# Performance work log

Measured on AMD Instinct MI355X. Metric: run time of the kernel, lower is better.

## Reference

```python
import jax, jax.numpy as jnp
import numpy as np
from jax import lax

B, T, IN, H, OUT = 64, 512, 256, 1024, 512

def _uniform(key, shape, std):
    return jax.random.uniform(key, shape, jnp.float32, -std, std)

def setup_inputs() -> dict:
    key = jax.random.key(0)
    ks = jax.random.split(key, 12)
    std = 1.0 / np.sqrt(H)
    return {
        "x": jax.random.normal(ks[0], (B, T, IN), jnp.float32),
        "Wx0": _uniform(ks[1], (H, IN), std), "bx0": _uniform(ks[2], (H,), std),
        "Wh0": _uniform(ks[3], (H, H), std),  "bh0": _uniform(ks[4], (H,), std),
        "Wx1": _uniform(ks[5], (H, H), std),  "bx1": _uniform(ks[6], (H,), std),
        "Wh1": _uniform(ks[7], (H, H), std),  "bh1": _uniform(ks[8], (H,), std),
        "Wfc": _uniform(ks[9], (OUT, H), 1.0 / np.sqrt(H)),
        "bfc": _uniform(ks[10], (OUT,), 1.0 / np.sqrt(H)),
    }

def _run_layer(xs, Wx, bx, Wh, bh):
    # xs: [B, T, D_in] -> hidden sequence [B, T, H]
    xproj = jnp.einsum('btd,hd->bth', xs, Wx) + bx + bh  # precompute input projection
    def step(h, xp):
        h = jnp.tanh(xp + h @ Wh.T)
        return h, h
    h0 = jnp.zeros((xs.shape[0], Wh.shape[0]), xs.dtype)
    _, hs = lax.scan(step, h0, jnp.swapaxes(xproj, 0, 1))  # [T, B, H]
    return jnp.swapaxes(hs, 0, 1)

def reference(x, Wx0, bx0, Wh0, bh0, Wx1, bx1, Wh1, bh1, Wfc, bfc):
    h1 = _run_layer(x, Wx0, bx0, Wh0, bh0)   # layer 0 hidden sequence
    h2 = _run_layer(h1, Wx1, bx1, Wh1, bh1)  # layer 1 hidden sequence
    last = h2[:, -1, :]                       # last timestep of top layer
    return last @ Wfc.T + bfc
```

## Files before the change

kernel.cpp:

```cpp
#include <hip/hip_runtime.h>
#include <hip/hip_bf16.h>

#define Bb   64
#define Tt   512
#define INN  256
#define HH   1024
#define OUTN 512

#define NCOL 32
#define MG   16
#define NGRP (Bb / MG)
#define NSLOT 64
#define FSTR 8

typedef __attribute__((ext_vector_type(8))) short bf16x8;
typedef __attribute__((ext_vector_type(4))) float f32x4;

__device__ __forceinline__ unsigned short f2b(float f) {
  unsigned u = __float_as_uint(f);
  u += 0x7FFFu + ((u >> 16) & 1u);
  return (unsigned short)(u >> 16);
}
__device__ __forceinline__ float b2f(unsigned short u) {
  return __uint_as_float((unsigned)u << 16);
}

__device__ __forceinline__ unsigned int cohLoadU32(const unsigned int* p) {
  return __hip_atomic_load(p, __ATOMIC_RELAXED, __HIP_MEMORY_SCOPE_AGENT);
}
__device__ __forceinline__ unsigned long long cohLoadU64(const unsigned long long* p) {
  return __hip_atomic_load(p, __ATOMIC_RELAXED, __HIP_MEMORY_SCOPE_AGENT);
}
__device__ __forceinline__ unsigned short cohLoadU16(const unsigned short* p) {
  return __hip_atomic_load(p, __ATOMIC_RELAXED, __HIP_MEMORY_SCOPE_AGENT);
}
__device__ __forceinline__ void cohStoreU16(unsigned short* p, unsigned short v) {
  __hip_atomic_store(p, v, __ATOMIC_RELAXED, __HIP_MEMORY_SCOPE_AGENT);
}
__device__ __forceinline__ void cohStoreU32(unsigned int* p, unsigned int v) {
  __hip_atomic_store(p, v, __ATOMIC_RELAXED, __HIP_MEMORY_SCOPE_AGENT);
}

__device__ __forceinline__ f32x4 splat4(float v) { f32x4 r = {v, v, v, v}; return r; }

union U16 { unsigned long long u[2]; bf16x8 v; };

#define ALOADO(d, p, OFF)                                                     \
  asm volatile("global_load_dwordx4 %0, %1, off offset:" #OFF " sc0 sc1"      \
               : "=v"(d) : "v"(p))
#define VMW(N)                                                                \
  do {                                                                        \
    asm volatile("s_waitcnt vmcnt(" #N ")" ::: "memory");                     \
    __builtin_amdgcn_sched_barrier(0);                                        \
  } while (0)

__global__ void cvt4(const float* __restrict__ in, unsigned short* __restrict__ out, int n4) {
  int i = blockIdx.x * blockDim.x + threadIdx.x;
  if (i >= n4) return;
  float4 v = ((const float4*)in)[i];
  ushort4 o;
  o.x = f2b(v.x); o.y = f2b(v.y); o.z = f2b(v.z); o.w = f2b(v.w);
  ((ushort4*)out)[i] = o;
}

__global__ void addv(const float* __restrict__ a, const float* __restrict__ b,
                     float* __restrict__ o, int n) {
  int i = blockIdx.x * blockDim.x + threadIdx.x;
  if (i < n) o[i] = a[i] + b[i];
}

__global__ void zerok(unsigned int* __restrict__ p, int n) {
  int i = blockIdx.x * blockDim.x + threadIdx.x;
  if (i < n) p[i] = 0u;
}

__device__ __forceinline__ void waitflags(const unsigned int* gf, int l, unsigned need) {
#pragma clang loop unroll(disable)
  for (int guard = 0; guard < 4000000; ++guard) {
    unsigned f = cohLoadU32(gf + l * FSTR);
    if (__all((int)(f >= need))) return;
    __builtin_amdgcn_s_sleep(1);
  }
}
__device__ __forceinline__ void waitflag1(const unsigned int* slot, unsigned need) {
#pragma clang loop unroll(disable)
  for (int guard = 0; guard < 4000000; ++guard) {
    if (cohLoadU32(slot) >= need) return;
    __builtin_amdgcn_s_sleep(1);
  }
}

#define ISSUE8(V, O0, O1, O2, O3, O4, O5, O6, O7)                             \
  ALOADO(V##0, Ap, O0); ALOADO(V##1, Ap, O1); ALOADO(V##2, Ap, O2);           \
  ALOADO(V##3, Ap, O3); ALOADO(V##4, Ap, O4); ALOADO(V##5, Ap, O5);           \
  ALOADO(V##6, Ap, O6); ALOADO(V##7, Ap, O7);
#define COMP8(V, WI)                                                          \
  acc  = __builtin_amdgcn_mfma_f32_16x16x32_bf16(V##0, w[(WI)+0], acc,  0,0,0);\
  acc2 = __builtin_amdgcn_mfma_f32_16x16x32_bf16(V##1, w[(WI)+1], acc2, 0,0,0);\
  acc  = __builtin_amdgcn_mfma_f32_16x16x32_bf16(V##2, w[(WI)+2], acc,  0,0,0);\
  acc2 = __builtin_amdgcn_mfma_f32_16x16x32_bf16(V##3, w[(WI)+3], acc2, 0,0,0);\
  acc  = __builtin_amdgcn_mfma_f32_16x16x32_bf16(V##4, w[(WI)+4], acc,  0,0,0);\
  acc2 = __builtin_amdgcn_mfma_f32_16x16x32_bf16(V##5, w[(WI)+5], acc2, 0,0,0);\
  acc  = __builtin_amdgcn_mfma_f32_16x16x32_bf16(V##6, w[(WI)+6], acc,  0,0,0);\
  acc2 = __builtin_amdgcn_mfma_f32_16x16x32_bf16(V##7, w[(WI)+7], acc2, 0,0,0);

__device__ __forceinline__ f32x4 kphase(const short* Ap, bf16x8* w, f32x4 acc) {
#pragma unroll
  for (int c = 0; c < 32; ++c) asm volatile("" : "+a"(w[c]));
  f32x4 acc2 = {0, 0, 0, 0};
  bf16x8 A_0, A_1, A_2, A_3, A_4, A_5, A_6, A_7;
  bf16x8 B_0, B_1, B_2, B_3, B_4, B_5, B_6, B_7;
  bf16x8 C_0, C_1, C_2, C_3, C_4, C_5, C_6, C_7;
  bf16x8 D_0, D_1, D_2, D_3, D_4, D_5, D_6, D_7;
  ISSUE8(A_,    0,   64,  128,  192,  256,  320,  384,  448)
  ISSUE8(B_,  512,  576,  640,  704,  768,  832,  896,  960)
  ISSUE8(C_, 1024, 1088, 1152, 1216, 1280, 1344, 1408, 1472)
  ISSUE8(D_, 1536, 1600, 1664, 1728, 1792, 1856, 1920, 1984)
  VMW(24); COMP8(A_,  0)
  VMW(16); COMP8(B_,  8)
  VMW(8);  COMP8(C_, 16)
  VMW(0);  COMP8(D_, 24)
  return acc + acc2;
}

__global__ __launch_bounds__(128) void rnn3(
    const __hip_bfloat16* __restrict__ xs,
    const __hip_bfloat16* __restrict__ Wx0, const __hip_bfloat16* __restrict__ Wh0,
    const __hip_bfloat16* __restrict__ Wx1, const __hip_bfloat16* __restrict__ Wh1,
    const float* __restrict__ b0s, const float* __restrict__ b1s,
    __hip_bfloat16* __restrict__ P0, __hip_bfloat16* __restrict__ P1,
    unsigned int* flags)
{
  const int tid = threadIdx.x;
  const int l   = tid & 63;
  const int wv  = tid >> 6;
  const int bid = blockIdx.x;
  const int stage = bid % 3;
  const int idx = bid / 3;
  const int j   = idx & 31;
  const int g   = idx >> 5;
  const int n0  = j * NCOL;
  const int rowA = g * MG;
  const int fr = l & 15;
  const int lh = l >> 4;
  const int rb = lh << 2;
  const int ccol = n0 + wv * 16 + fr;

  unsigned int* gf0 = flags + (0 * NGRP + g) * (NSLOT * FSTR);
  unsigned int* gfx = flags + (1 * NGRP + g) * (NSLOT * FSTR);
  unsigned int* gf1 = flags + (2 * NGRP + g) * (NSLOT * FSTR);
  const int wslot = (j * 2 + wv) * FSTR;
  const long laneA = (long)(rowA + fr) * HH + (lh << 3);
  unsigned short* P0u = (unsigned short*)P0;
  unsigned short* P1u = (unsigned short*)P1;

  const short* Wg = (const short*)(stage == 0 ? Wh0 : (stage == 1 ? Wx1 : Wh1));
  const short* Wgrow = Wg + (long)ccol * HH + (lh << 3);
  bf16x8 w[32];
#pragma unroll
  for (int c = 0; c < 32; ++c) w[c] = *(const bf16x8*)(Wgrow + (c << 5));
#pragma unroll
  for (int c = 0; c < 32; ++c) asm volatile("" : "+a"(w[c]));

  if (stage == 0) {
    const float bias = b0s[ccol];
    const short* xrow = (const short*)xs + (long)(rowA + fr) * (Tt * INN) + (lh << 3);
    const short* Wx0row = (const short*)Wx0 + (long)ccol * INN + (lh << 3);
    bf16x8 wx[8];
#pragma unroll
    for (int c = 0; c < 8; ++c) wx[c] = *(const bf16x8*)(Wx0row + (c << 5));
#pragma unroll
    for (int c = 0; c < 8; ++c) asm volatile("" : "+a"(wx[c]));
    f32x4 acc = splat4(bias);
#pragma unroll
    for (int c = 0; c < 8; ++c) {
      bf16x8 a = *(const bf16x8*)(xrow + (c << 5));
      acc = __builtin_amdgcn_mfma_f32_16x16x32_bf16(a, wx[c], acc, 0, 0, 0);
    }
    for (int t = 0; t < Tt; ++t) {
      if (t > 0) {
        waitflags(gf0, l, (unsigned)t);
        acc = kphase((const short*)P0 + (long)(t - 1) * (Bb * HH) + laneA, w, acc);
      }
      const long cb = ((long)t * Bb + rowA + rb) * HH + ccol;
#pragma unroll
      for (int r = 0; r < 4; ++r)
        cohStoreU16(P0u + cb + (long)r * HH, f2b(tanhf(acc[r])));
      asm volatile("s_waitcnt vmcnt(0)" ::: "memory");
      if (l == 0) cohStoreU32(gf0 + wslot, (unsigned)(t + 1));
      if (t + 1 < Tt) {
        acc = splat4(bias);
        const short* xr = xrow + (t + 1) * INN;
#pragma unroll
        for (int c = 0; c < 8; ++c) {
          bf16x8 a = *(const bf16x8*)(xr + (c << 5));
          acc = __builtin_amdgcn_mfma_f32_16x16x32_bf16(a, wx[c], acc, 0, 0, 0);
        }
      }
    }
  } else if (stage == 1) {
    const float bias = b1s[ccol];
    for (int t = 0; t < Tt; ++t) {
      waitflags(gf0, l, (unsigned)(t + 1));
      f32x4 acc = kphase((const short*)P0 + (long)t * (Bb * HH) + laneA, w,
                         splat4(bias));
      const long cb = ((long)t * Bb + rowA + rb) * HH + ccol;
#pragma unroll
      for (int r = 0; r < 4; ++r)
        cohStoreU16(P1u + cb + (long)r * HH, f2b(acc[r]));
      asm volatile("s_waitcnt vmcnt(0)" ::: "memory");
      if (l == 0) cohStoreU32(gfx + wslot, (unsigned)(t + 1));
    }
  } else {
    const unsigned int* myxpf = gfx + wslot;
    for (int t = 0; t < Tt; ++t) {
      waitflag1(myxpf, (unsigned)(t + 1));
      const long cb = ((long)t * Bb + rowA + rb) * HH + ccol;
      float xb[4];
#pragma unroll
      for (int r = 0; r < 4; ++r)
        xb[r] = b2f(cohLoadU16(P1u + cb + (long)r * HH));
      f32x4 acc = {0, 0, 0, 0};
      if (t > 0) {
        waitflags(gf1, l, (unsigned)t);
        acc = kphase((const short*)P1 + (long)(t - 1) * (Bb * HH) + laneA, w, acc);
      }
#pragma unroll
      for (int r = 0; r < 4; ++r)
        cohStoreU16(P1u + cb + (long)r * HH, f2b(tanhf(acc[r] + xb[r])));
      asm volatile("s_waitcnt vmcnt(0)" ::: "memory");
      if (l == 0) cohStoreU32(gf1 + wslot, (unsigned)(t + 1));
    }
  }
}

__global__ void fc_kernel(const __hip_bfloat16* __restrict__ A,
                          const __hip_bfloat16* __restrict__ W,
                          const float* __restrict__ bias,
                          float* __restrict__ C)
{
  const int l   = threadIdx.x;
  const int m0  = blockIdx.x << 4;
  const int n0  = blockIdx.y << 6;
  const int r16 = l & 15;
  const int lh  = l >> 4;

  const unsigned long long* Au =
      (const unsigned long long*)((const short*)A + (long)(m0 + r16) * HH);
  const short* Wp = (const short*)W;
  const long w0 = (long)(n0 + r16) * HH + (lh << 3);
  const long wS = (long)HH << 4;

  f32x4 acc0 = {0,0,0,0}, acc1 = {0,0,0,0}, acc2 = {0,0,0,0}, acc3 = {0,0,0,0};
  for (int kc = 0; kc < HH; kc += 32) {
    U16 a;
    a.u[0] = cohLoadU64(Au + (kc >> 2) + (lh << 1));
    a.u[1] = cohLoadU64(Au + (kc >> 2) + (lh << 1) + 1);
    bf16x8 b0 = *(const bf16x8*)(Wp + w0 +          kc);
    bf16x8 b1 = *(const bf16x8*)(Wp + w0 + wS     + kc);
    bf16x8 b2 = *(const bf16x8*)(Wp + w0 + 2 * wS + kc);
    bf16x8 b3 = *(const bf16x8*)(Wp + w0 + 3 * wS + kc);
    acc0 = __builtin_amdgcn_mfma_f32_16x16x32_bf16(a.v, b0, acc0, 0, 0, 0);
    acc1 = __builtin_amdgcn_mfma_f32_16x16x32_bf16(a.v, b1, acc1, 0, 0, 0);
    acc2 = __builtin_amdgcn_mfma_f32_16x16x32_bf16(a.v, b2, acc2, 0, 0, 0);
    acc3 = __builtin_amdgcn_mfma_f32_16x16x32_bf16(a.v, b3, acc3, 0, 0, 0);
  }
  const int col = l & 15;
  const int rbb = (l >> 4) << 2;
#define FCEP(FIDX, ACC)                                                       \
  { const int n = n0 + (FIDX << 4) + col;                                     \
    _Pragma("unroll")                                                         \
    for (int r = 0; r < 4; ++r)                                               \
      C[(long)(m0 + rbb + r) * OUTN + n] = ACC[r] + bias[n]; }
  FCEP(0, acc0) FCEP(1, acc1) FCEP(2, acc2) FCEP(3, acc3)
#undef FCEP
}

extern "C" void kernel_launch(void* const* d_in, const int* in_sizes, int n_in,
                              void* d_out, int out_size, void* d_ws, size_t ws_size,
                              hipStream_t stream)
{
  const float* x   = (const float*)d_in[0];
  const float* Wx0 = (const float*)d_in[1];
  const float* bx0 = (const float*)d_in[2];
  const float* Wh0 = (const float*)d_in[3];
  const float* bh0 = (const float*)d_in[4];
  const float* Wx1 = (const float*)d_in[5];
  const float* bx1 = (const float*)d_in[6];
  const float* Wh1 = (const float*)d_in[7];
  const float* bh1 = (const float*)d_in[8];
  const float* Wfc = (const float*)d_in[9];
  const float* bfc = (const float*)d_in[10];

  char* ws = (char*)d_ws;
  const long SZ_XBF = (long)Bb * Tt * INN * 2;
  const long SZ_P   = (long)Bb * Tt * HH  * 2;
  __hip_bfloat16* xbf   = (__hip_bfloat16*)(ws);
  __hip_bfloat16* P0    = (__hip_bfloat16*)(ws + SZ_XBF);
  __hip_bfloat16* P1    = (__hip_bfloat16*)(ws + SZ_XBF + SZ_P);
  __hip_bfloat16* Wx0b  = (__hip_bfloat16*)(ws + SZ_XBF + 2 * SZ_P);
  __hip_bfloat16* Wh0b  = (__hip_bfloat16*)((char*)Wx0b + (long)HH * INN * 2);
  __hip_bfloat16* Wx1b  = (__hip_bfloat16*)((char*)Wh0b + (long)HH * HH * 2);
  __hip_bfloat16* Wh1b  = (__hip_bfloat16*)((char*)Wx1b + (long)HH * HH * 2);
  __hip_bfloat16* Wfcb  = (__hip_bfloat16*)((char*)Wh1b + (long)HH * HH * 2);
  float*          b0sum = (float*)((char*)Wfcb + (long)OUTN * HH * 2);
  float*          b1sum = (float*)((char*)b0sum + HH * 4);
  unsigned int*   flg   = (unsigned int*)((char*)b1sum + HH * 4);

  const int FLGN = 3 * NGRP * NSLOT * FSTR;

  {
    int n4;
    n4 = (Bb * Tt * INN) / 4; cvt4<<<(n4 + 255) / 256, 256, 0, stream>>>(x,   (unsigned short*)xbf,  n4);
    n4 = (HH * INN) / 4;      cvt4<<<(n4 + 255) / 256, 256, 0, stream>>>(Wx0, (unsigned short*)Wx0b, n4);
    n4 = (HH * HH) / 4;       cvt4<<<(n4 + 255) / 256, 256, 0, stream>>>(Wh0, (unsigned short*)Wh0b, n4);
    n4 = (HH * HH) / 4;       cvt4<<<(n4 + 255) / 256, 256, 0, stream>>>(Wx1, (unsigned short*)Wx1b, n4);
    n4 = (HH * HH) / 4;       cvt4<<<(n4 + 255) / 256, 256, 0, stream>>>(Wh1, (unsigned short*)Wh1b, n4);
    n4 = (OUTN * HH) / 4;     cvt4<<<(n4 + 255) / 256, 256, 0, stream>>>(Wfc, (unsigned short*)Wfcb, n4);
    addv<<<4, 256, 0, stream>>>(bx0, bh0, b0sum, HH);
    addv<<<4, 256, 0, stream>>>(bx1, bh1, b1sum, HH);
    zerok<<<(FLGN + 255) / 256, 256, 0, stream>>>(flg, FLGN);
  }

  rnn3<<<dim3(384), 128, 0, stream>>>(
      xbf, Wx0b, Wh0b, Wx1b, Wh1b, b0sum, b1sum, P0, P1, flg);

  fc_kernel<<<dim3(Bb / 16, OUTN / 64), 64, 0, stream>>>(
      P1 + (long)(Tt - 1) * Bb * HH, Wfcb, bfc, (float*)d_out);
}
```

Measured before the change: 3.349 ms.

## Widen each wave to 32 output columns, halving the persistent block count

Each wave now computes two 16-column tiles (left and right) and reuses every loaded A fragment for two MFMAs, so it keeps 64 weight fragments resident in AGPRs instead of 32. The grid shrinks from 384 to 192 persistent blocks, the flag slots per group drop to 32, and the wait loops poll only 32 flags. The Wx0 weights are now reloaded from memory on each step rather than kept in registers. The intent is to halve the redundant hidden-state reads and the flag traffic per step. The cost is a longer serial MFMA chain per wave, heavier register pressure, and fewer CUs working on each timestep.

```diff
diff --git a/kernel.cpp b/kernel.cpp
--- a/kernel.cpp
+++ b/kernel.cpp
@@ -7,11 +7,11 @@
 #define HH   1024
 #define OUTN 512
 
-#define NCOL 32
-#define MG   16
-#define NGRP (Bb / MG)
-#define NSLOT 64
-#define FSTR 8
+#define MG    16
+#define NGRP  (Bb / MG)
+#define NBLKG 16
+#define NSLOT 32
+#define FSTR  8
 
 typedef __attribute__((ext_vector_type(8))) short bf16x8;
 typedef __attribute__((ext_vector_type(4))) float f32x4;
@@ -77,7 +77,7 @@
 __device__ __forceinline__ void waitflags(const unsigned int* gf, int l, unsigned need) {
 #pragma clang loop unroll(disable)
   for (int guard = 0; guard < 4000000; ++guard) {
-    unsigned f = cohLoadU32(gf + l * FSTR);
+    unsigned f = cohLoadU32(gf + (l & 31) * FSTR);
     if (__all((int)(f >= need))) return;
     __builtin_amdgcn_s_sleep(1);
   }
@@ -94,20 +94,17 @@
   ALOADO(V##0, Ap, O0); ALOADO(V##1, Ap, O1); ALOADO(V##2, Ap, O2);           \
   ALOADO(V##3, Ap, O3); ALOADO(V##4, Ap, O4); ALOADO(V##5, Ap, O5);           \
   ALOADO(V##6, Ap, O6); ALOADO(V##7, Ap, O7);
+#define C2(V, CH)                                                             \
+  accL = __builtin_amdgcn_mfma_f32_16x16x32_bf16(V, w[2*(CH)],   accL, 0,0,0);\
+  accR = __builtin_amdgcn_mfma_f32_16x16x32_bf16(V, w[2*(CH)+1], accR, 0,0,0);
 #define COMP8(V, WI)                                                          \
-  acc  = __builtin_amdgcn_mfma_f32_16x16x32_bf16(V##0, w[(WI)+0], acc,  0,0,0);\
-  acc2 = __builtin_amdgcn_mfma_f32_16x16x32_bf16(V##1, w[(WI)+1], acc2, 0,0,0);\
-  acc  = __builtin_amdgcn_mfma_f32_16x16x32_bf16(V##2, w[(WI)+2], acc,  0,0,0);\
-  acc2 = __builtin_amdgcn_mfma_f32_16x16x32_bf16(V##3, w[(WI)+3], acc2, 0,0,0);\
-  acc  = __builtin_amdgcn_mfma_f32_16x16x32_bf16(V##4, w[(WI)+4], acc,  0,0,0);\
-  acc2 = __builtin_amdgcn_mfma_f32_16x16x32_bf16(V##5, w[(WI)+5], acc2, 0,0,0);\
-  acc  = __builtin_amdgcn_mfma_f32_16x16x32_bf16(V##6, w[(WI)+6], acc,  0,0,0);\
-  acc2 = __builtin_amdgcn_mfma_f32_16x16x32_bf16(V##7, w[(WI)+7], acc2, 0,0,0);
-
-__device__ __forceinline__ f32x4 kphase(const short* Ap, bf16x8* w, f32x4 acc) {
-#pragma unroll
-  for (int c = 0; c < 32; ++c) asm volatile("" : "+a"(w[c]));
-  f32x4 acc2 = {0, 0, 0, 0};
+  C2(V##0, (WI)+0) C2(V##1, (WI)+1) C2(V##2, (WI)+2) C2(V##3, (WI)+3)         \
+  C2(V##4, (WI)+4) C2(V##5, (WI)+5) C2(V##6, (WI)+6) C2(V##7, (WI)+7)
+
+__device__ __forceinline__ void kphase32(const short* Ap, bf16x8* w,
+                                         f32x4& accL, f32x4& accR) {
+#pragma unroll
+  for (int c = 0; c < 64; ++c) asm volatile("" : "+a"(w[c]));
   bf16x8 A_0, A_1, A_2, A_3, A_4, A_5, A_6, A_7;
   bf16x8 B_0, B_1, B_2, B_3, B_4, B_5, B_6, B_7;
   bf16x8 C_0, C_1, C_2, C_3, C_4, C_5, C_6, C_7;
@@ -120,7 +117,6 @@
   VMW(16); COMP8(B_,  8)
   VMW(8);  COMP8(C_, 16)
   VMW(0);  COMP8(D_, 24)
-  return acc + acc2;
 }
 
 __global__ __launch_bounds__(128) void rnn3(
@@ -137,14 +133,15 @@
   const int bid = blockIdx.x;
   const int stage = bid % 3;
   const int idx = bid / 3;
-  const int j   = idx & 31;
-  const int g   = idx >> 5;
-  const int n0  = j * NCOL;
+  const int j   = idx & 15;
+  const int g   = idx >> 4;
+  const int n0  = j * 64 + wv * 32;
   const int rowA = g * MG;
   const int fr = l & 15;
   const int lh = l >> 4;
   const int rb = lh << 2;
-  const int ccol = n0 + wv * 16 + fr;
+  const int colL = n0 + fr;
+  const int colR = colL + 16;
 
   unsigned int* gf0 = flags + (0 * NGRP + g) * (NSLOT * FSTR);
   unsigned int* gfx = flags + (1 * NGRP + g) * (NSLOT * FSTR);
@@ -155,59 +152,65 @@
   unsigned short* P1u = (unsigned short*)P1;
 
   const short* Wg = (const short*)(stage == 0 ? Wh0 : (stage == 1 ? Wx1 : Wh1));
-  const short* Wgrow = Wg + (long)ccol * HH + (lh << 3);
-  bf16x8 w[32];
-#pragma unroll
-  for (int c = 0; c < 32; ++c) w[c] = *(const bf16x8*)(Wgrow + (c << 5));
-#pragma unroll
-  for (int c = 0; c < 32; ++c) asm volatile("" : "+a"(w[c]));
+  const short* WrowL = Wg + (long)colL * HH + (lh << 3);
+  const short* WrowR = WrowL + 16 * HH;
+  bf16x8 w[64];
+#pragma unroll
+  for (int c = 0; c < 32; ++c) {
+    w[2 * c]     = *(const bf16x8*)(WrowL + (c << 5));
+    w[2 * c + 1] = *(const bf16x8*)(WrowR + (c << 5));
+  }
+#pragma unroll
+  for (int c = 0; c < 64; ++c) asm volatile("" : "+a"(w[c]));
 
   if (stage == 0) {
-    const float bias = b0s[ccol];
+    const float biasL = b0s[colL], biasR = b0s[colR];
     const short* xrow = (const short*)xs + (long)(rowA + fr) * (Tt * INN) + (lh << 3);
-    const short* Wx0row = (const short*)Wx0 + (long)ccol * INN + (lh << 3);
-    bf16x8 wx[8];
-#pragma unroll
-    for (int c = 0; c < 8; ++c) wx[c] = *(const bf16x8*)(Wx0row + (c << 5));
-#pragma unroll
-    for (int c = 0; c < 8; ++c) asm volatile("" : "+a"(wx[c]));
-    f32x4 acc = splat4(bias);
+    const short* WxL = (const short*)Wx0 + (long)colL * INN + (lh << 3);
+    const short* WxR = WxL + 16 * INN;
+    f32x4 accL = splat4(biasL), accR = splat4(biasR);
 #pragma unroll
     for (int c = 0; c < 8; ++c) {
       bf16x8 a = *(const bf16x8*)(xrow + (c << 5));
-      acc = __builtin_amdgcn_mfma_f32_16x16x32_bf16(a, wx[c], acc, 0, 0, 0);
+      accL = __builtin_amdgcn_mfma_f32_16x16x32_bf16(a, *(const bf16x8*)(WxL + (c << 5)), accL, 0, 0, 0);
+      accR = __builtin_amdgcn_mfma_f32_16x16x32_bf16(a, *(const bf16x8*)(WxR + (c << 5)), accR, 0, 0, 0);
     }
     for (int t = 0; t < Tt; ++t) {
       if (t > 0) {
         waitflags(gf0, l, (unsigned)t);
-        acc = kphase((const short*)P0 + (long)(t - 1) * (Bb * HH) + laneA, w, acc);
-      }
-      const long cb = ((long)t * Bb + rowA + rb) * HH + ccol;
-#pragma unroll
-      for (int r = 0; r < 4; ++r)
-        cohStoreU16(P0u + cb + (long)r * HH, f2b(tanhf(acc[r])));
+        kphase32((const short*)P0 + (long)(t - 1) * (Bb * HH) + laneA, w, accL, accR);
+      }
+      const long cb = ((long)t * Bb + rowA + rb) * HH + colL;
+#pragma unroll
+      for (int r = 0; r < 4; ++r) {
+        cohStoreU16(P0u + cb + (long)r * HH,      f2b(tanhf(accL[r])));
+        cohStoreU16(P0u + cb + (long)r * HH + 16, f2b(tanhf(accR[r])));
+      }
       asm volatile("s_waitcnt vmcnt(0)" ::: "memory");
       if (l == 0) cohStoreU32(gf0 + wslot, (unsigned)(t + 1));
       if (t + 1 < Tt) {
-        acc = splat4(bias);
+        accL = splat4(biasL); accR = splat4(biasR);
         const short* xr = xrow + (t + 1) * INN;
 #pragma unroll
         for (int c = 0; c < 8; ++c) {
           bf16x8 a = *(const bf16x8*)(xr + (c << 5));
-          acc = __builtin_amdgcn_mfma_f32_16x16x32_bf16(a, wx[c], acc, 0, 0, 0);
+          accL = __builtin_amdgcn_mfma_f32_16x16x32_bf16(a, *(const bf16x8*)(WxL + (c << 5)), accL, 0, 0, 0);
+          accR = __builtin_amdgcn_mfma_f32_16x16x32_bf16(a, *(const bf16x8*)(WxR + (c << 5)), accR, 0, 0, 0);
         }
       }
     }
   } else if (stage == 1) {
-    const float bias = b1s[ccol];
+    const float biasL = b1s[colL], biasR = b1s[colR];
     for (int t = 0; t < Tt; ++t) {
       waitflags(gf0, l, (unsigned)(t + 1));
-      f32x4 acc = kphase((const short*)P0 + (long)t * (Bb * HH) + laneA, w,
-                         splat4(bias));
-      const long cb = ((long)t * Bb + rowA + rb) * HH + ccol;
-#pragma unroll
-      for (int r = 0; r < 4; ++r)
-        cohStoreU16(P1u + cb + (long)r * HH, f2b(acc[r]));
+      f32x4 accL = splat4(biasL), accR = splat4(biasR);
+      kphase32((const short*)P0 + (long)t * (Bb * HH) + laneA, w, accL, accR);
+      const long cb = ((long)t * Bb + rowA + rb) * HH + colL;
+#pragma unroll
+      for (int r = 0; r < 4; ++r) {
+        cohStoreU16(P1u + cb + (long)r * HH,      f2b(accL[r]));
+        cohStoreU16(P1u + cb + (long)r * HH + 16, f2b(accR[r]));
+      }
       asm volatile("s_waitcnt vmcnt(0)" ::: "memory");
       if (l == 0) cohStoreU32(gfx + wslot, (unsigned)(t + 1));
     }
@@ -215,19 +218,23 @@
     const unsigned int* myxpf = gfx + wslot;
     for (int t = 0; t < Tt; ++t) {
       waitflag1(myxpf, (unsigned)(t + 1));
-      const long cb = ((long)t * Bb + rowA + rb) * HH + ccol;
-      float xb[4];
-#pragma unroll
-      for (int r = 0; r < 4; ++r)
-        xb[r] = b2f(cohLoadU16(P1u + cb + (long)r * HH));
-      f32x4 acc = {0, 0, 0, 0};
+      const long cb = ((long)t * Bb + rowA + rb) * HH + colL;
+      float xbL[4], xbR[4];
+#pragma unroll
+      for (int r = 0; r < 4; ++r) {
+        xbL[r] = b2f(cohLoadU16(P1u + cb + (long)r * HH));
+        xbR[r] = b2f(cohLoadU16(P1u + cb + (long)r * HH + 16));
+      }
+      f32x4 accL = {0, 0, 0, 0}, accR = {0, 0, 0, 0};
       if (t > 0) {
         waitflags(gf1, l, (unsigned)t);
-        acc = kphase((const short*)P1 + (long)(t - 1) * (Bb * HH) + laneA, w, acc);
-      }
-#pragma unroll
-      for (int r = 0; r < 4; ++r)
-        cohStoreU16(P1u + cb + (long)r * HH, f2b(tanhf(acc[r] + xb[r])));
+        kphase32((const short*)P1 + (long)(t - 1) * (Bb * HH) + laneA, w, accL, accR);
+      }
+#pragma unroll
+      for (int r = 0; r < 4; ++r) {
+        cohStoreU16(P1u + cb + (long)r * HH,      f2b(tanhf(accL[r] + xbL[r])));
+        cohStoreU16(P1u + cb + (long)r * HH + 16, f2b(tanhf(accR[r] + xbR[r])));
+      }
       asm volatile("s_waitcnt vmcnt(0)" ::: "memory");
       if (l == 0) cohStoreU32(gf1 + wslot, (unsigned)(t + 1));
     }
@@ -322,7 +329,7 @@
     zerok<<<(FLGN + 255) / 256, 256, 0, stream>>>(flg, FLGN);
   }
 
-  rnn3<<<dim3(384), 128, 0, stream>>>(
+  rnn3<<<dim3(3 * NGRP * NBLKG), 128, 0, stream>>>(
       xbf, Wx0b, Wh0b, Wx1b, Wh1b, b0sum, b1sum, P0, P1, flg);
 
   fc_kernel<<<dim3(Bb / 16, OUTN / 64), 64, 0, stream>>>(
```

After: 4.626 ms. 1.38x slower.
